# Optimization experiments

Hardware: AMD Instinct MI355X
Metric: run time of the kernel (lower is better)

## Reference

```python
import jax, jax.numpy as jnp
import numpy as np

N = 20000      # nodes
E = 160000     # edges
F_IN = 128     # num_node_features
D = 128        # embedding_size (out_channels)
H = 4          # heads
NEG = 0.2      # GATv2Conv negative_slope
N_LAYERS = 3


def setup_inputs() -> dict:
    key = jax.random.key(0)
    ks = jax.random.split(key, 12)
    s = 0.05
    return {
        "x": jax.random.normal(ks[0], (N, F_IN), jnp.float32),
        "edge_index": jax.random.randint(ks[1], (2, E), 0, N, jnp.int64),
        "edge_attr": jax.random.normal(ks[2], (E, 2), jnp.float32),
        "Wf": jax.random.normal(ks[3], (F_IN, D), jnp.float32) * s,
        "bf": jnp.zeros((D,), jnp.float32),
        "Wl": jax.random.normal(ks[4], (D, H * D), jnp.float32) * s,
        "bl": jnp.zeros((H * D,), jnp.float32),
        "Wr": jax.random.normal(ks[5], (D, H * D), jnp.float32) * s,
        "br": jnp.zeros((H * D,), jnp.float32),
        "We": jax.random.normal(ks[6], (2, H * D), jnp.float32) * s,
        "att": jax.random.normal(ks[7], (H, D), jnp.float32) * s,
        "bias_out": jnp.zeros((D,), jnp.float32),
    }


def reference(x, edge_index, edge_attr, Wf, bf, Wl, bl, Wr, br, We, att, bias_out):
    src, dst = edge_index[0], edge_index[1]

    # add_self_loops with fill_value='mean': self-loop edge_attr = mean of
    # incoming edge_attr per node (0 where a node has no incoming edges)
    ea_sum = jax.ops.segment_sum(edge_attr, dst, num_segments=N)            # [N,2]
    cnt = jax.ops.segment_sum(jnp.ones((E,), edge_attr.dtype), dst, num_segments=N)
    loop_attr = ea_sum / jnp.maximum(cnt, 1.0)[:, None]
    loop_idx = jnp.arange(N, dtype=src.dtype)
    fsrc = jnp.concatenate([src, loop_idx])                                  # [E+N]
    fdst = jnp.concatenate([dst, loop_idx])
    fea = jnp.concatenate([edge_attr, loop_attr], axis=0)                    # [E+N,2]

    ee = (fea @ We).reshape(-1, H, D)                                        # [E+N,H,D]

    def gatv2_layer(h):
        xl = (h @ Wl + bl).reshape(N, H, D)   # lin_l -> source-side / message
        xr = (h @ Wr + br).reshape(N, H, D)   # lin_r -> target-side
        e = jax.nn.leaky_relu(xl[fsrc] + xr[fdst] + ee, NEG)                 # [E+N,H,D]
        logits = jnp.einsum('ehd,hd->eh', e, att)                            # [E+N,H]
        m = jax.ops.segment_max(logits, fdst, num_segments=N)                # [N,H]
        w = jnp.exp(logits - m[fdst])
        denom = jax.ops.segment_sum(w, fdst, num_segments=N)                 # [N,H]
        alpha = w / denom[fdst]                                              # segment softmax
        msg = xl[fsrc] * alpha[..., None]                                    # [E+N,H,D]
        out = jax.ops.segment_sum(msg, fdst, num_segments=N)                 # [N,H,D]
        return out.mean(axis=1) + bias_out                                   # concat=False

    h = x @ Wf + bf
    for _ in range(N_LAYERS):
        h = jax.nn.leaky_relu(gatv2_layer(h), 0.01)  # F.leaky_relu default slope
    return h
```

## Files before the change

kernel.cpp:

```cpp
#include <hip/hip_runtime.h>
#include <hip/hip_bf16.h>

#define NN 20000
#define NE 160000
#define EF (NE + NN)
#define DD 128
#define HH 4
#define NPA (NN * DD)
#define NPW (1024 * 128 + 128 * 128 + 1024)
#define DEGB ((NE + 255) / 256)
#define NBLK 40

typedef unsigned short u16;
typedef unsigned int u32;

using short8  = __attribute__((ext_vector_type(8))) short;
using ushort8 = __attribute__((ext_vector_type(8))) unsigned short;
using float4v = __attribute__((ext_vector_type(4))) float;
using f32x2   = __attribute__((ext_vector_type(2))) float;

__device__ __forceinline__ float bf2f(u16 u) {
    union { u32 i; float f; } c;
    c.i = ((u32)u) << 16;
    return c.f;
}
__device__ __forceinline__ u16 f2bf(float f) {
    union { float f; u32 u; } c;
    c.f = f;
    u32 u = c.u;
    u32 r = (u + 0x7fffu + ((u >> 16) & 1u)) >> 16;
    return (u16)r;
}

template<int CTRL>
__device__ __forceinline__ float dpp_add(float v) {
    int t = __builtin_amdgcn_update_dpp(0, __builtin_bit_cast(int, v),
                                        CTRL, 0xf, 0xf, true);
    return v + __builtin_bit_cast(float, t);
}

__device__ __forceinline__ void gld16(const void* g, void* l) {
    __builtin_amdgcn_global_load_lds(
        (const __attribute__((address_space(1))) unsigned int*)g,
        (__attribute__((address_space(3))) unsigned int*)l,
        16, 0, 0);
}


__global__ void k_zero_f(float* __restrict__ p, int n) {
    int i = blockIdx.x * blockDim.x + threadIdx.x;
    if (i < n) p[i] = 0.f;
}


__global__ void k_degpack(const int* __restrict__ ei, const float* __restrict__ ea,
                          const float* __restrict__ x,
                          const float* __restrict__ Wl, const float* __restrict__ Wr,
                          const float* __restrict__ bl, const float* __restrict__ br,
                          const float* __restrict__ Wf,
                          int* __restrict__ cnt, float* __restrict__ ea_sum,
                          u16* __restrict__ Axh, u16* __restrict__ Axl,
                          u16* __restrict__ W2Th, u16* __restrict__ W2Tl,
                          u16* __restrict__ WfTh, u16* __restrict__ WfTl,
                          float* __restrict__ bias2) {
    int gb = blockIdx.x;
    if (gb < DEGB) {
        int e = gb * 256 + threadIdx.x;
        if (e >= NE) return;
        int t = ei[NE + e];
        atomicAdd(&cnt[t], 1);
        atomicAdd(&ea_sum[t * 2 + 0], ea[e * 2 + 0]);
        atomicAdd(&ea_sum[t * 2 + 1], ea[e * 2 + 1]);
        return;
    }
    int i = (gb - DEGB) * 256 + threadIdx.x;
    if (i < NPA) {
        float a = x[i];
        u16 h = f2bf(a);
        Axh[i] = h;
        Axl[i] = f2bf(a - bf2f(h));
        return;
    }
    i -= NPA;
    if (i < 1024 * 128) {
        int n = i >> 7, k = i & 127;
        float w = (n < 512) ? Wl[k * 512 + n] : Wr[k * 512 + (n - 512)];
        u16 h = f2bf(w);
        W2Th[n * 128 + k] = h;
        W2Tl[n * 128 + k] = f2bf(w - bf2f(h));
    } else if (i < 1024 * 128 + 128 * 128) {
        int u = i - 1024 * 128;
        int n = u >> 7, k = u & 127;
        float w = Wf[k * 128 + n];
        u16 h = f2bf(w);
        WfTh[n * 128 + k] = h;
        WfTl[n * 128 + k] = f2bf(w - bf2f(h));
    } else if (i < NPW) {
        int n = i - (1024 * 128 + 128 * 128);
        bias2[n] = (n < 512) ? bl[n] : br[n - 512];
    }
}


__global__ __launch_bounds__(512) void k_scan_a(const int* __restrict__ cnt,
                                                int* __restrict__ rowptr,
                                                int* __restrict__ bsum) {
    __shared__ int ws[8];
    int tid = threadIdx.x;
    int i = blockIdx.x * 512 + tid;
    int l = tid & 63, w = tid >> 6;
    int v = (i < NN) ? (cnt[i] + 1) : 0;
    #pragma unroll
    for (int off = 1; off < 64; off <<= 1) {
        int u = __shfl_up(v, off, 64);
        if (l >= off) v += u;
    }
    if (l == 63) ws[w] = v;
    __syncthreads();
    if (w == 0) {
        int s = (l < 8) ? ws[l] : 0;
        #pragma unroll
        for (int off = 1; off < 8; off <<= 1) {
            int u = __shfl_up(s, off, 64);
            if (l >= off) s += u;
        }
        if (l < 8) ws[l] = s;
    }
    __syncthreads();
    v += (w > 0) ? ws[w - 1] : 0;
    if (i < NN) rowptr[i + 1] = v;
    if (tid == 511) bsum[blockIdx.x] = v;
}

__global__ void k_scan_c(int* __restrict__ rowptr, const int* __restrict__ bsum) {
    int l = threadIdx.x & 63;
    int v = (l < NBLK) ? bsum[l] : 0;
    #pragma unroll
    for (int off = 1; off < 64; off <<= 1) {
        int u = __shfl_up(v, off, 64);
        if (l >= off) v += u;
    }
    int i = blockIdx.x * blockDim.x + threadIdx.x;
    int j = i >> 9;
    int off = (j > 0) ? __shfl(v, j - 1, 64) : 0;
    if (i < NN) rowptr[i + 1] += off;
    if (i == 0) rowptr[0] = 0;
}


__global__ void k_fill(const int* __restrict__ ei, const float* __restrict__ ea,
                       const int* __restrict__ rowptr, int* __restrict__ fillc,
                       const int* __restrict__ cnt, const float* __restrict__ ea_sum,
                       int* __restrict__ srcs,
                       float* __restrict__ fa0, float* __restrict__ fa1) {
    int e = blockIdx.x * blockDim.x + threadIdx.x;
    if (e < NE) {
        int s = ei[e], t = ei[NE + e];
        int pos = atomicAdd(&fillc[t], 1);
        int slot = rowptr[t] + pos;
        srcs[slot] = s;
        fa0[slot] = ea[e * 2];
        fa1[slot] = ea[e * 2 + 1];
    } else if (e < NE + NN) {
        int n = e - NE;
        int slot = rowptr[n + 1] - 1;
        srcs[slot] = n;
        float c = fmaxf((float)cnt[n], 1.f);
        fa0[slot] = ea_sum[n * 2 + 0] / c;
        fa1[slot] = ea_sum[n * 2 + 1] / c;
    }
}


template<int SPLIT, int NB>
__global__ __launch_bounds__(256, 3) void k_mgemm(
        const u16* __restrict__ Ahg, const u16* __restrict__ Alg,
        const u16* __restrict__ BTh, const u16* __restrict__ BTl,
        const float* __restrict__ bias, float* __restrict__ C1,
        u16* __restrict__ C2b,
        u16* __restrict__ Oh, u16* __restrict__ Ol, int M) {
    __shared__ u16 sAh[64 * 128], sBh[64 * 128], sBl[64 * 128];
    int m0 = blockIdx.y * 64;
    int t = threadIdx.x;
    int lane = t & 63;
    int wm = (t >> 6) & 1;
    int wn = t >> 7;
    int fm = lane & 15;
    int q8 = (lane >> 4) * 8;

    short8 fal[4][2];
    #pragma unroll
    for (int i = 0; i < 2; ++i) {
        const u16* p = Alg + (size_t)(m0 + wm * 32 + i * 16 + fm) * 128 + q8;
        #pragma unroll
        for (int kk = 0; kk < 4; ++kk)
            fal[kk][i] = *(const short8*)(p + kk * 32);
    }

    #pragma unroll
    for (int i = 0; i < 4; ++i) {
        int cb = (t & 192) + 256 * i;
        int c = cb + lane;
        int row = c >> 4, ch = c & 15;
        int gm = m0 + row;
        if (gm >= M) gm = M - 1;
        gld16(&Ahg[(size_t)gm * 128 + ((ch ^ (row & 15)) << 3)], &sAh[cb * 8]);
    }

    int cq = q8 >> 3;

    for (int bb = 0; bb < NB; ++bb) {
        int n0 = (blockIdx.x * NB + bb) * 64;
        __syncthreads();
        #pragma unroll
        for (int i = 0; i < 4; ++i) {
            int cb = (t & 192) + 256 * i;
            int c = cb + lane;
            int row = c >> 4, ch = c & 15;
            size_t gofs = (size_t)(n0 + row) * 128 + ((ch ^ (row & 15)) << 3);
            gld16(&BTh[gofs], &sBh[cb * 8]);
            gld16(&BTl[gofs], &sBl[cb * 8]);
        }
        __syncthreads();

        float4v zz = {0.f, 0.f, 0.f, 0.f};
        float4v acc[2][2];
        acc[0][0] = zz; acc[0][1] = zz; acc[1][0] = zz; acc[1][1] = zz;

        #pragma unroll
        for (int k0 = 0; k0 < 128; k0 += 32) {
            int cl = (k0 >> 3) + cq;
            int sw = (cl ^ fm) << 3;
            short8 fah[2], fbh[2], fbl[2];
            #pragma unroll
            for (int i = 0; i < 2; ++i) {
                int mr = wm * 32 + i * 16 + fm;
                fah[i] = *(const short8*)&sAh[mr * 128 + sw];
                int nr = wn * 32 + i * 16 + fm;
                fbh[i] = *(const short8*)&sBh[nr * 128 + sw];
                fbl[i] = *(const short8*)&sBl[nr * 128 + sw];
            }
            #pragma unroll
            for (int i = 0; i < 2; ++i)
                #pragma unroll
                for (int j = 0; j < 2; ++j) {
                    acc[i][j] = __builtin_amdgcn_mfma_f32_16x16x32_bf16(fah[i], fbh[j], acc[i][j], 0, 0, 0);
                    acc[i][j] = __builtin_amdgcn_mfma_f32_16x16x32_bf16(fah[i], fbl[j], acc[i][j], 0, 0, 0);
                    acc[i][j] = __builtin_amdgcn_mfma_f32_16x16x32_bf16(fal[k0 >> 5][i], fbh[j], acc[i][j], 0, 0, 0);
                }
        }

        #pragma unroll
        for (int i = 0; i < 2; ++i) {
            #pragma unroll
            for (int j = 0; j < 2; ++j) {
                int gn = n0 + wn * 32 + j * 16 + fm;
                float bv = bias[gn];
                #pragma unroll
                for (int r = 0; r < 4; ++r) {
                    int gm = m0 + wm * 32 + i * 16 + (lane >> 4) * 4 + r;
                    if (gm < M) {
                        float v = acc[i][j][r] + bv;
                        if (SPLIT) {
                            u16 h = f2bf(v);
                            Oh[gm * 128 + gn] = h;
                            Ol[gm * 128 + gn] = f2bf(v - bf2f(h));
                        } else if (n0 < 512) {
                            C1[gm * 512 + gn] = v;
                        } else {
                            C2b[gm * 512 + gn - 512] = f2bf(v);
                        }
                    }
                }
            }
        }
    }
}


__global__ __launch_bounds__(128) void k_gat(
        const int* __restrict__ rowptr, const int* __restrict__ srcs,
        const float* __restrict__ fa0, const float* __restrict__ fa1,
        const float* __restrict__ xl, const u16* __restrict__ xr,
        const float* __restrict__ We, const float* __restrict__ att,
        const float* __restrict__ bias_out,
        u16* __restrict__ Oh, u16* __restrict__ Ol,
        float* __restrict__ outp, int last) {
    __shared__ float sacc[512];
    __shared__ float sden[4];
    int half = threadIdx.x >> 6;
    int n = blockIdx.x;
    int l = threadIdx.x & 63;
    int d0 = l * 8;

    f32x2 xr2[4], we0p[4], we1p[4], at6p[4], at4p[4];
    {
        ushort8 u = *reinterpret_cast<const ushort8*>(&xr[(size_t)n * 512 + d0]);
        #pragma unroll
        for (int k = 0; k < 4; ++k) {
            f32x2 t; t.x = bf2f(u[2 * k]); t.y = bf2f(u[2 * k + 1]);
            xr2[k] = t;
        }
        const f32x2* w0 = reinterpret_cast<const f32x2*>(&We[d0]);
        const f32x2* w1 = reinterpret_cast<const f32x2*>(&We[512 + d0]);
        const f32x2* av = reinterpret_cast<const f32x2*>(&att[d0]);
        #pragma unroll
        for (int k = 0; k < 4; ++k) {
            we0p[k] = w0[k];
            we1p[k] = w1[k];
            f32x2 a = av[k];
            at6p[k] = a * 0.6f;
            at4p[k] = a * 0.4f;
        }
    }

    int b0 = rowptr[n], b1 = rowptr[n + 1];
    int nit = (b1 - b0 - half + 1) >> 1;

    int sv = 0, f0i = 0, f1i = 0;
    {
        int me = b0 + half + 2 * l;
        if (l < nit) {
            sv  = srcs[me];
            f0i = __builtin_bit_cast(int, fa0[me]);
            f1i = __builtin_bit_cast(int, fa1[me]);
        }
    }

    f32x2 acc2[4];
    acc2[0] = f32x2{0.f, 0.f}; acc2[1] = f32x2{0.f, 0.f};
    acc2[2] = f32x2{0.f, 0.f}; acc2[3] = f32x2{0.f, 0.f};
    float den = 0.f;

    auto body = [&](float4 A, float4 B, float f0, float f1) {
        f32x2 f0p; f0p.x = f0; f0p.y = f0;
        f32x2 f1p; f1p.x = f1; f1p.y = f1;
        f32x2 xv2[4];
        xv2[0].x = A.x; xv2[0].y = A.y;
        xv2[1].x = A.z; xv2[1].y = A.w;
        xv2[2].x = B.x; xv2[2].y = B.y;
        xv2[3].x = B.z; xv2[3].y = B.w;
        f32x2 p2 = {0.f, 0.f};
        #pragma unroll
        for (int k = 0; k < 4; ++k) {
            f32x2 t = __builtin_elementwise_fma(f0p, we0p[k], xr2[k]);
            t = __builtin_elementwise_fma(f1p, we1p[k], t);
            f32x2 v2 = xv2[k] + t;
            f32x2 a2 = __builtin_elementwise_abs(v2);
            p2 = __builtin_elementwise_fma(at6p[k], v2, p2);
            p2 = __builtin_elementwise_fma(at4p[k], a2, p2);
        }
        float p = p2.x + p2.y;
        p = dpp_add<0xB1>(p);
        p = dpp_add<0x4E>(p);
        p = dpp_add<0x124>(p);
        p = dpp_add<0x128>(p);
        float wt = __expf(p);
        den += wt;
        f32x2 wtp; wtp.x = wt; wtp.y = wt;
        #pragma unroll
        for (int k = 0; k < 4; ++k)
            acc2[k] = __builtin_elementwise_fma(wtp, xv2[k], acc2[k]);
    };

    int nfast = nit < 64 ? nit : 64;
    #pragma unroll 4
    for (int it = 0; it < nfast; ++it) {
        int   s  = __builtin_amdgcn_readlane(sv, it);
        float f0 = __builtin_bit_cast(float, __builtin_amdgcn_readlane(f0i, it));
        float f1 = __builtin_bit_cast(float, __builtin_amdgcn_readlane(f1i, it));
        const float* xp = &xl[(size_t)s * 512 + d0];
        float4 A = *reinterpret_cast<const float4*>(xp);
        float4 B = *reinterpret_cast<const float4*>(xp + 4);
        body(A, B, f0, f1);
    }
    for (int e = b0 + half + 128; e < b1; e += 2) {
        int s = srcs[e];
        const float* xp = &xl[(size_t)s * 512 + d0];
        float4 A = *reinterpret_cast<const float4*>(xp);
        float4 B = *reinterpret_cast<const float4*>(xp + 4);
        body(A, B, fa0[e], fa1[e]);
    }

    if (half == 1) {
        *reinterpret_cast<float4*>(&sacc[d0]) =
            make_float4(acc2[0].x, acc2[0].y, acc2[1].x, acc2[1].y);
        *reinterpret_cast<float4*>(&sacc[d0 + 4]) =
            make_float4(acc2[2].x, acc2[2].y, acc2[3].x, acc2[3].y);
        if ((l & 15) == 0) sden[l >> 4] = den;
    }
    __syncthreads();
    if (half == 1) return;
    float acc[8] = {acc2[0].x, acc2[0].y, acc2[1].x, acc2[1].y,
                    acc2[2].x, acc2[2].y, acc2[3].x, acc2[3].y};
    #pragma unroll
    for (int k = 0; k < 8; ++k) acc[k] += sacc[d0 + k];
    den += sden[l >> 4];
    float inv = 1.f / den;
    float val[8];
    #pragma unroll
    for (int k = 0; k < 8; ++k) {
        float v = acc[k] * inv;
        v += __shfl_xor(v, 16, 64);
        v += __shfl_xor(v, 32, 64);
        val[k] = v;
    }
    if (l < 16) {
        #pragma unroll
        for (int k = 0; k < 8; ++k) {
            float v = val[k] * 0.25f + bias_out[d0 + k];
            v = v > 0.f ? v : 0.01f * v;
            val[k] = v;
        }
        if (last) {
            #pragma unroll
            for (int k = 0; k < 8; ++k) outp[n * 128 + d0 + k] = val[k];
        } else {
            #pragma unroll
            for (int k = 0; k < 8; ++k) {
                u16 hv = f2bf(val[k]);
                Oh[n * 128 + d0 + k] = hv;
                Ol[n * 128 + d0 + k] = f2bf(val[k] - bf2f(hv));
            }
        }
    }
}


extern "C" void kernel_launch(void* const* d_in, const int* in_sizes, int n_in,
                              void* d_out, int out_size, void* d_ws, size_t ws_size,
                              hipStream_t stream) {
    size_t o = 0;
    auto alloc = [&](size_t bytes) { size_t cur = o; o += (bytes + 255) & ~(size_t)255; return cur; };
    size_t off_cnt    = alloc((size_t)NN * 4);
    size_t off_fillc  = alloc((size_t)NN * 4);
    size_t off_easum  = alloc((size_t)NN * 2 * 4);
    size_t off_rowptr = alloc((size_t)(NN + 1) * 4);
    size_t off_bsum   = alloc((size_t)NBLK * 4);
    size_t off_srcs   = alloc((size_t)EF * 4);
    size_t off_fa0    = alloc((size_t)EF * 4);
    size_t off_fa1    = alloc((size_t)EF * 4);
    size_t off_axh    = alloc((size_t)NN * DD * 2);
    size_t off_axl    = alloc((size_t)NN * DD * 2);
    size_t off_ah     = alloc((size_t)NN * DD * 2);
    size_t off_al     = alloc((size_t)NN * DD * 2);
    size_t off_xl     = alloc((size_t)NN * 512 * 4);
    size_t off_xr     = alloc((size_t)NN * 512 * 2);
    size_t off_w2th   = alloc((size_t)1024 * 128 * 2);
    size_t off_w2tl   = alloc((size_t)1024 * 128 * 2);
    size_t off_wfth   = alloc((size_t)128 * 128 * 2);
    size_t off_wftl   = alloc((size_t)128 * 128 * 2);
    size_t off_bias2  = alloc((size_t)1024 * 4);
    size_t need = o;

    bool ok = (n_in == 12) && d_ws != nullptr && ws_size >= need
           && out_size == NN * DD
           && in_sizes[0] == NN * DD && in_sizes[1] == 2 * NE
           && in_sizes[2] == NE * 2 && in_sizes[3] == 128 * 128
           && in_sizes[5] == 128 * 512 && in_sizes[9] == 2 * 512
           && in_sizes[10] == 4 * 128 && in_sizes[11] == 128;
    if (!ok) {
        k_zero_f<<<(NN * DD + 255) / 256, 256, 0, stream>>>((float*)d_out, NN * DD);
        return;
    }

    const float* x        = (const float*)d_in[0];
    const int*   ei       = (const int*)d_in[1];
    const float* ea       = (const float*)d_in[2];
    const float* Wf       = (const float*)d_in[3];
    const float* bf       = (const float*)d_in[4];
    const float* Wl       = (const float*)d_in[5];
    const float* bl       = (const float*)d_in[6];
    const float* Wr       = (const float*)d_in[7];
    const float* br       = (const float*)d_in[8];
    const float* We       = (const float*)d_in[9];
    const float* att      = (const float*)d_in[10];
    const float* bias_out = (const float*)d_in[11];

    char* base = (char*)d_ws;
    int*   cnt    = (int*)(base + off_cnt);
    int*   fillc  = (int*)(base + off_fillc);
    float* ea_sum = (float*)(base + off_easum);
    int*   rowptr = (int*)(base + off_rowptr);
    int*   bsum   = (int*)(base + off_bsum);
    int*   srcs   = (int*)(base + off_srcs);
    float* fa0    = (float*)(base + off_fa0);
    float* fa1    = (float*)(base + off_fa1);
    u16*   Axh    = (u16*)(base + off_axh);
    u16*   Axl    = (u16*)(base + off_axl);
    u16*   Ah     = (u16*)(base + off_ah);
    u16*   Al     = (u16*)(base + off_al);
    float* xl     = (float*)(base + off_xl);
    u16*   xr     = (u16*)(base + off_xr);
    u16*   W2Th   = (u16*)(base + off_w2th);
    u16*   W2Tl   = (u16*)(base + off_w2tl);
    u16*   WfTh   = (u16*)(base + off_wfth);
    u16*   WfTl   = (u16*)(base + off_wftl);
    float* bias2  = (float*)(base + off_bias2);

    size_t zero_bytes = off_easum + (size_t)NN * 2 * 4 - off_cnt;
    hipMemsetAsync(cnt, 0, zero_bytes, stream);

    int packb = (NPA + NPW + 255) / 256;
    k_degpack<<<DEGB + packb, 256, 0, stream>>>(ei, ea, x, Wl, Wr, bl, br, Wf,
                                                cnt, ea_sum, Axh, Axl,
                                                W2Th, W2Tl, WfTh, WfTl, bias2);
    k_scan_a<<<NBLK, 512, 0, stream>>>(cnt, rowptr, bsum);
    k_scan_c<<<(NN + 255) / 256, 256, 0, stream>>>(rowptr, bsum);
    k_fill<<<(NE + NN + 255) / 256, 256, 0, stream>>>(ei, ea, rowptr, fillc,
                                                      cnt, ea_sum, srcs, fa0, fa1);

    const int MT = (NN + 63) / 64;
    k_mgemm<1, 2><<<dim3(1, MT), 256, 0, stream>>>(Axh, Axl, WfTh, WfTl,
                                                   bf, nullptr, nullptr, Ah, Al, NN);

    for (int layer = 0; layer < 3; ++layer) {
        k_mgemm<0, 8><<<dim3(2, MT), 256, 0, stream>>>(Ah, Al, W2Th, W2Tl,
                                                       bias2, xl, xr, nullptr, nullptr, NN);
        int last = (layer == 2);
        k_gat<<<NN, 128, 0, stream>>>(rowptr, srcs, fa0, fa1, xl, xr,
                                      We, att, bias_out, Ah, Al,
                                      (float*)d_out, last);
    }
}
```

Measured before the change: 396.4 us.

## Load GEMM operand fragments directly from global memory, dropping LDS staging

The split-bf16 MFMA GEMM no longer stages A and B tiles in shared memory through global_load_lds with barriers. Each wave now loads its own A high/low and B high/low fragments straight from global into registers. The layer GEMM grid is also widened from 2 to 4 column blocks, with 4 N-tiles per block instead of 8. This removes LDS traffic and syncs but adds redundant global/L2 reads and register pressure, and reloads A in twice as many blocks.

Result: slower. 508.8 us (+28.4%).

```diff
diff --git a/kernel.cpp b/kernel.cpp
--- a/kernel.cpp
+++ b/kernel.cpp
@@ -37,13 +37,6 @@
     int t = __builtin_amdgcn_update_dpp(0, __builtin_bit_cast(int, v),
                                         CTRL, 0xf, 0xf, true);
     return v + __builtin_bit_cast(float, t);
-}
-
-__device__ __forceinline__ void gld16(const void* g, void* l) {
-    __builtin_amdgcn_global_load_lds(
-        (const __attribute__((address_space(1))) unsigned int*)g,
-        (__attribute__((address_space(3))) unsigned int*)l,
-        16, 0, 0);
 }
 
 
@@ -179,7 +172,6 @@
         const float* __restrict__ bias, float* __restrict__ C1,
         u16* __restrict__ C2b,
         u16* __restrict__ Oh, u16* __restrict__ Ol, int M) {
-    __shared__ u16 sAh[64 * 128], sBh[64 * 128], sBl[64 * 128];
     int m0 = blockIdx.y * 64;
     int t = threadIdx.x;
     int lane = t & 63;
@@ -188,67 +180,51 @@
     int fm = lane & 15;
     int q8 = (lane >> 4) * 8;
 
-    short8 fal[4][2];
+    short8 fah[4][2], fal[4][2];
     #pragma unroll
     for (int i = 0; i < 2; ++i) {
-        const u16* p = Alg + (size_t)(m0 + wm * 32 + i * 16 + fm) * 128 + q8;
-        #pragma unroll
-        for (int kk = 0; kk < 4; ++kk)
-            fal[kk][i] = *(const short8*)(p + kk * 32);
+        int gm = m0 + wm * 32 + i * 16 + fm;
+        if (gm > M - 1) gm = M - 1;
+        const u16* ph = Ahg + (size_t)gm * 128 + q8;
+        const u16* pl = Alg + (size_t)gm * 128 + q8;
+        #pragma unroll
+        for (int kk = 0; kk < 4; ++kk) {
+            fah[kk][i] = *(const short8*)(ph + kk * 32);
+            fal[kk][i] = *(const short8*)(pl + kk * 32);
+        }
     }
 
     #pragma unroll
-    for (int i = 0; i < 4; ++i) {
-        int cb = (t & 192) + 256 * i;
-        int c = cb + lane;
-        int row = c >> 4, ch = c & 15;
-        int gm = m0 + row;
-        if (gm >= M) gm = M - 1;
-        gld16(&Ahg[(size_t)gm * 128 + ((ch ^ (row & 15)) << 3)], &sAh[cb * 8]);
-    }
-
-    int cq = q8 >> 3;
-
     for (int bb = 0; bb < NB; ++bb) {
         int n0 = (blockIdx.x * NB + bb) * 64;
-        __syncthreads();
-        #pragma unroll
-        for (int i = 0; i < 4; ++i) {
-            int cb = (t & 192) + 256 * i;
-            int c = cb + lane;
-            int row = c >> 4, ch = c & 15;
-            size_t gofs = (size_t)(n0 + row) * 128 + ((ch ^ (row & 15)) << 3);
-            gld16(&BTh[gofs], &sBh[cb * 8]);
-            gld16(&BTl[gofs], &sBl[cb * 8]);
-        }
-        __syncthreads();
+
+        short8 fbh[4][2], fbl[4][2];
+        #pragma unroll
+        for (int j = 0; j < 2; ++j) {
+            int gn = n0 + wn * 32 + j * 16 + fm;
+            const u16* ph = BTh + (size_t)gn * 128 + q8;
+            const u16* pl = BTl + (size_t)gn * 128 + q8;
+            #pragma unroll
+            for (int kk = 0; kk < 4; ++kk) {
+                fbh[kk][j] = *(const short8*)(ph + kk * 32);
+                fbl[kk][j] = *(const short8*)(pl + kk * 32);
+            }
+        }
 
         float4v zz = {0.f, 0.f, 0.f, 0.f};
         float4v acc[2][2];
         acc[0][0] = zz; acc[0][1] = zz; acc[1][0] = zz; acc[1][1] = zz;
 
         #pragma unroll
-        for (int k0 = 0; k0 < 128; k0 += 32) {
-            int cl = (k0 >> 3) + cq;
-            int sw = (cl ^ fm) << 3;
-            short8 fah[2], fbh[2], fbl[2];
-            #pragma unroll
-            for (int i = 0; i < 2; ++i) {
-                int mr = wm * 32 + i * 16 + fm;
-                fah[i] = *(const short8*)&sAh[mr * 128 + sw];
-                int nr = wn * 32 + i * 16 + fm;
-                fbh[i] = *(const short8*)&sBh[nr * 128 + sw];
-                fbl[i] = *(const short8*)&sBl[nr * 128 + sw];
-            }
+        for (int kk = 0; kk < 4; ++kk)
             #pragma unroll
             for (int i = 0; i < 2; ++i)
                 #pragma unroll
                 for (int j = 0; j < 2; ++j) {
-                    acc[i][j] = __builtin_amdgcn_mfma_f32_16x16x32_bf16(fah[i], fbh[j], acc[i][j], 0, 0, 0);
-                    acc[i][j] = __builtin_amdgcn_mfma_f32_16x16x32_bf16(fah[i], fbl[j], acc[i][j], 0, 0, 0);
-                    acc[i][j] = __builtin_amdgcn_mfma_f32_16x16x32_bf16(fal[k0 >> 5][i], fbh[j], acc[i][j], 0, 0, 0);
+                    acc[i][j] = __builtin_amdgcn_mfma_f32_16x16x32_bf16(fah[kk][i], fbh[kk][j], acc[i][j], 0, 0, 0);
+                    acc[i][j] = __builtin_amdgcn_mfma_f32_16x16x32_bf16(fah[kk][i], fbl[kk][j], acc[i][j], 0, 0, 0);
+                    acc[i][j] = __builtin_amdgcn_mfma_f32_16x16x32_bf16(fal[kk][i], fbh[kk][j], acc[i][j], 0, 0, 0);
                 }
-        }
 
         #pragma unroll
         for (int i = 0; i < 2; ++i) {
@@ -515,7 +491,7 @@
                                                    bf, nullptr, nullptr, Ah, Al, NN);
 
     for (int layer = 0; layer < 3; ++layer) {
-        k_mgemm<0, 8><<<dim3(2, MT), 256, 0, stream>>>(Ah, Al, W2Th, W2Tl,
+        k_mgemm<0, 4><<<dim3(4, MT), 256, 0, stream>>>(Ah, Al, W2Th, W2Tl,
                                                        bias2, xl, xr, nullptr, nullptr, NN);
         int last = (layer == 2);
         k_gat<<<NN, 128, 0, stream>>>(rowptr, srcs, fa0, fa1, xl, xr,
```

## Prefetch next B tile into registers while computing current tile in GEMM

Applied to the files above, without the earlier changes.

Replaces the direct global-to-LDS loads of each B tile, which sat between two barriers, with register-staged loads. The next tile's global loads are issued before the MFMA work on the current tile, then written to LDS after it. This is meant to hide global memory latency behind compute. In exchange it uses more VGPRs (16 short8 registers), which may lower occupancy, and it no longer uses the direct-to-LDS load path.

Result: no change. 401.2 us (+1.2%).

```diff
diff --git a/kernel.cpp b/kernel.cpp
--- a/kernel.cpp
+++ b/kernel.cpp
@@ -207,22 +207,47 @@
         gld16(&Ahg[(size_t)gm * 128 + ((ch ^ (row & 15)) << 3)], &sAh[cb * 8]);
     }
 
+    int brow[4], bgc[4], bdofs[4];
+    #pragma unroll
+    for (int i = 0; i < 4; ++i) {
+        int c = t + 256 * i;
+        int row = c >> 4, ch = c & 15;
+        brow[i] = row;
+        bgc[i] = ch * 8;
+        bdofs[i] = row * 128 + ((ch ^ (row & 15)) << 3);
+    }
+
+    short8 rbh[4], rbl[4];
+    {
+        int n0 = blockIdx.x * NB * 64;
+        #pragma unroll
+        for (int i = 0; i < 4; ++i) {
+            size_t g = (size_t)(n0 + brow[i]) * 128 + bgc[i];
+            rbh[i] = *(const short8*)&BTh[g];
+            rbl[i] = *(const short8*)&BTl[g];
+        }
+    }
+    #pragma unroll
+    for (int i = 0; i < 4; ++i) {
+        *(short8*)&sBh[bdofs[i]] = rbh[i];
+        *(short8*)&sBl[bdofs[i]] = rbl[i];
+    }
+    __syncthreads();
+
     int cq = q8 >> 3;
 
     for (int bb = 0; bb < NB; ++bb) {
+        if (bb + 1 < NB) {
+            int n1 = (blockIdx.x * NB + bb + 1) * 64;
+            #pragma unroll
+            for (int i = 0; i < 4; ++i) {
+                size_t g = (size_t)(n1 + brow[i]) * 128 + bgc[i];
+                rbh[i] = *(const short8*)&BTh[g];
+                rbl[i] = *(const short8*)&BTl[g];
+            }
+        }
+
         int n0 = (blockIdx.x * NB + bb) * 64;
-        __syncthreads();
-        #pragma unroll
-        for (int i = 0; i < 4; ++i) {
-            int cb = (t & 192) + 256 * i;
-            int c = cb + lane;
-            int row = c >> 4, ch = c & 15;
-            size_t gofs = (size_t)(n0 + row) * 128 + ((ch ^ (row & 15)) << 3);
-            gld16(&BTh[gofs], &sBh[cb * 8]);
-            gld16(&BTl[gofs], &sBl[cb * 8]);
-        }
-        __syncthreads();
-
         float4v zz = {0.f, 0.f, 0.f, 0.f};
         float4v acc[2][2];
         acc[0][0] = zz; acc[0][1] = zz; acc[1][0] = zz; acc[1][1] = zz;
@@ -273,6 +298,16 @@
                     }
                 }
             }
+        }
+
+        if (bb + 1 < NB) {
+            __syncthreads();
+            #pragma unroll
+            for (int i = 0; i < 4; ++i) {
+                *(short8*)&sBh[bdofs[i]] = rbh[i];
+                *(short8*)&sBl[bdofs[i]] = rbl[i];
+            }
+            __syncthreads();
         }
     }
 }
```

## Fold input projection Wf into first layer's Wl/Wr weights

Applied to the files above, without the earlier changes.

Precomputes the composed weight Wf·[Wl|Wr] and composed bias in a small kernel, so layer 0's GEMM takes x directly and the separate x@Wf GEMM with its split-bf16 output is removed. This saves one full N×128 GEMM launch plus the writing and re-reading of the intermediate h. It adds a small serial weight-composition kernel whose per-thread loop of 128 strided loads may be slow, and it changes rounding slightly because the composed weights are split into bf16 hi/lo.

After: 400.2 us. About the same (+1.0%).

```diff
diff --git a/kernel.cpp b/kernel.cpp
--- a/kernel.cpp
+++ b/kernel.cpp
@@ -7,7 +7,7 @@
 #define DD 128
 #define HH 4
 #define NPA (NN * DD)
-#define NPW (1024 * 128 + 128 * 128 + 1024)
+#define NPW (1024 * 128 + 1024)
 #define DEGB ((NE + 255) / 256)
 #define NBLK 40
 
@@ -53,15 +53,38 @@
 }
 
 
+__global__ void k_compose(const float* __restrict__ Wf,
+                          const float* __restrict__ Wl, const float* __restrict__ Wr,
+                          const float* __restrict__ bf,
+                          const float* __restrict__ bl, const float* __restrict__ br,
+                          u16* __restrict__ WcTh, u16* __restrict__ WcTl,
+                          float* __restrict__ biasc) {
+    int idx = blockIdx.x * 256 + threadIdx.x;
+    int n = idx >> 7, f = idx & 127;
+    const float* col = (n < 512) ? &Wl[n] : &Wr[n - 512];
+    float s = 0.f;
+    #pragma unroll 4
+    for (int d = 0; d < 128; ++d)
+        s = fmaf(Wf[f * 128 + d], col[d * 512], s);
+    u16 h = f2bf(s);
+    WcTh[n * 128 + f] = h;
+    WcTl[n * 128 + f] = f2bf(s - bf2f(h));
+    if (f == 0) {
+        float b = (n < 512) ? bl[n] : br[n - 512];
+        for (int d = 0; d < 128; ++d)
+            b = fmaf(bf[d], col[d * 512], b);
+        biasc[n] = b;
+    }
+}
+
+
 __global__ void k_degpack(const int* __restrict__ ei, const float* __restrict__ ea,
                           const float* __restrict__ x,
                           const float* __restrict__ Wl, const float* __restrict__ Wr,
                           const float* __restrict__ bl, const float* __restrict__ br,
-                          const float* __restrict__ Wf,
                           int* __restrict__ cnt, float* __restrict__ ea_sum,
                           u16* __restrict__ Axh, u16* __restrict__ Axl,
                           u16* __restrict__ W2Th, u16* __restrict__ W2Tl,
-                          u16* __restrict__ WfTh, u16* __restrict__ WfTl,
                           float* __restrict__ bias2) {
     int gb = blockIdx.x;
     if (gb < DEGB) {
@@ -88,15 +111,8 @@
         u16 h = f2bf(w);
         W2Th[n * 128 + k] = h;
         W2Tl[n * 128 + k] = f2bf(w - bf2f(h));
-    } else if (i < 1024 * 128 + 128 * 128) {
-        int u = i - 1024 * 128;
-        int n = u >> 7, k = u & 127;
-        float w = Wf[k * 128 + n];
-        u16 h = f2bf(w);
-        WfTh[n * 128 + k] = h;
-        WfTl[n * 128 + k] = f2bf(w - bf2f(h));
     } else if (i < NPW) {
-        int n = i - (1024 * 128 + 128 * 128);
+        int n = i - 1024 * 128;
         bias2[n] = (n < 512) ? bl[n] : br[n - 512];
     }
 }
@@ -172,13 +188,12 @@
 }
 
 
-template<int SPLIT, int NB>
+template<int NB>
 __global__ __launch_bounds__(256, 3) void k_mgemm(
         const u16* __restrict__ Ahg, const u16* __restrict__ Alg,
         const u16* __restrict__ BTh, const u16* __restrict__ BTl,
         const float* __restrict__ bias, float* __restrict__ C1,
-        u16* __restrict__ C2b,
-        u16* __restrict__ Oh, u16* __restrict__ Ol, int M) {
+        u16* __restrict__ C2b, int M) {
     __shared__ u16 sAh[64 * 128], sBh[64 * 128], sBl[64 * 128];
     int m0 = blockIdx.y * 64;
     int t = threadIdx.x;
@@ -261,11 +276,7 @@
                     int gm = m0 + wm * 32 + i * 16 + (lane >> 4) * 4 + r;
                     if (gm < M) {
                         float v = acc[i][j][r] + bv;
-                        if (SPLIT) {
-                            u16 h = f2bf(v);
-                            Oh[gm * 128 + gn] = h;
-                            Ol[gm * 128 + gn] = f2bf(v - bf2f(h));
-                        } else if (n0 < 512) {
+                        if (n0 < 512) {
                             C1[gm * 512 + gn] = v;
                         } else {
                             C2b[gm * 512 + gn - 512] = f2bf(v);
@@ -448,9 +459,10 @@
     size_t off_xr     = alloc((size_t)NN * 512 * 2);
     size_t off_w2th   = alloc((size_t)1024 * 128 * 2);
     size_t off_w2tl   = alloc((size_t)1024 * 128 * 2);
-    size_t off_wfth   = alloc((size_t)128 * 128 * 2);
-    size_t off_wftl   = alloc((size_t)128 * 128 * 2);
+    size_t off_wcth   = alloc((size_t)1024 * 128 * 2);
+    size_t off_wctl   = alloc((size_t)1024 * 128 * 2);
     size_t off_bias2  = alloc((size_t)1024 * 4);
+    size_t off_biasc  = alloc((size_t)1024 * 4);
     size_t need = o;
 
     bool ok = (n_in == 12) && d_ws != nullptr && ws_size >= need
@@ -494,29 +506,34 @@
     u16*   xr     = (u16*)(base + off_xr);
     u16*   W2Th   = (u16*)(base + off_w2th);
     u16*   W2Tl   = (u16*)(base + off_w2tl);
-    u16*   WfTh   = (u16*)(base + off_wfth);
-    u16*   WfTl   = (u16*)(base + off_wftl);
+    u16*   WcTh   = (u16*)(base + off_wcth);
+    u16*   WcTl   = (u16*)(base + off_wctl);
     float* bias2  = (float*)(base + off_bias2);
+    float* biasc  = (float*)(base + off_biasc);
 
     size_t zero_bytes = off_easum + (size_t)NN * 2 * 4 - off_cnt;
     hipMemsetAsync(cnt, 0, zero_bytes, stream);
 
+    k_compose<<<512, 256, 0, stream>>>(Wf, Wl, Wr, bf, bl, br, WcTh, WcTl, biasc);
+
     int packb = (NPA + NPW + 255) / 256;
-    k_degpack<<<DEGB + packb, 256, 0, stream>>>(ei, ea, x, Wl, Wr, bl, br, Wf,
+    k_degpack<<<DEGB + packb, 256, 0, stream>>>(ei, ea, x, Wl, Wr, bl, br,
                                                 cnt, ea_sum, Axh, Axl,
-                                                W2Th, W2Tl, WfTh, WfTl, bias2);
+                                                W2Th, W2Tl, bias2);
     k_scan_a<<<NBLK, 512, 0, stream>>>(cnt, rowptr, bsum);
     k_scan_c<<<(NN + 255) / 256, 256, 0, stream>>>(rowptr, bsum);
     k_fill<<<(NE + NN + 255) / 256, 256, 0, stream>>>(ei, ea, rowptr, fillc,
                                                       cnt, ea_sum, srcs, fa0, fa1);
 
     const int MT = (NN + 63) / 64;
-    k_mgemm<1, 2><<<dim3(1, MT), 256, 0, stream>>>(Axh, Axl, WfTh, WfTl,
-                                                   bf, nullptr, nullptr, Ah, Al, NN);
-
     for (int layer = 0; layer < 3; ++layer) {
-        k_mgemm<0, 8><<<dim3(2, MT), 256, 0, stream>>>(Ah, Al, W2Th, W2Tl,
-                                                       bias2, xl, xr, nullptr, nullptr, NN);
+        const u16*   Ahp = (layer == 0) ? Axh  : Ah;
+        const u16*   Alp = (layer == 0) ? Axl  : Al;
+        const u16*   Bhp = (layer == 0) ? WcTh : W2Th;
+        const u16*   Blp = (layer == 0) ? WcTl : W2Tl;
+        const float* bp  = (layer == 0) ? biasc : bias2;
+        k_mgemm<8><<<dim3(2, MT), 256, 0, stream>>>(Ahp, Alp, Bhp, Blp,
+                                                    bp, xl, xr, NN);
         int last = (layer == 2);
         k_gat<<<NN, 128, 0, stream>>>(rowptr, srcs, fa0, fa1, xl, xr,
                                       We, att, bias_out, Ah, Al,
```
